# Optimization experiments

Measured on AMD Instinct MI355X. Metric: run time of the kernel, lower is better.

The kernel has to match this reference:

```python
import jax, jax.numpy as jnp
import numpy as np

B, S, V, H, NL, NH, FF, L = 32, 256, 30522, 768, 12, 12, 3072, 9
DH = H // NH
SCALE = 1.0 / float(np.sqrt(DH))

def _ln(x, g, b, eps=1e-12):
    mu = x.mean(-1, keepdims=True)
    var = ((x - mu) ** 2).mean(-1, keepdims=True)
    return (x - mu) * jax.lax.rsqrt(var + eps) * g + b

def _crf_nll(em, tags, mask, start, end, trans):
    # em: [B,S,L] log-softmaxed emissions; tags: [B,S] int; mask: [B,S] bool
    b, s, l = em.shape
    bi = jnp.arange(b)
    em_t = jnp.swapaxes(em, 0, 1)          # [S,B,L]
    tg_t = tags.T                           # [S,B]
    m_t = mask.T.astype(em.dtype)           # [S,B]
    # numerator: score of the gold path
    score0 = start[tags[:, 0]] + em[bi, 0, tags[:, 0]]
    def num_step(sc, xs):
        e, tg, tgp, m = xs
        return sc + m * (trans[tgp, tg] + e[bi, tg]), None
    num, _ = jax.lax.scan(num_step, score0, (em_t[1:], tg_t[1:], tg_t[:-1], m_t[1:]))
    seq_ends = mask.sum(1).astype(jnp.int32) - 1
    num = num + end[tags[bi, seq_ends]]
    # denominator: log partition via forward algorithm
    alpha0 = start[None, :] + em[:, 0]      # [B,L]
    def den_step(al, xs):
        e, m = xs
        new = jax.nn.logsumexp(al[:, :, None] + trans[None] + e[:, None, :], axis=1)
        return jnp.where(m[:, None] > 0, new, al), None
    alpha, _ = jax.lax.scan(den_step, alpha0, (em_t[1:], m_t[1:]))
    den = jax.nn.logsumexp(alpha + end[None, :], axis=1)
    return -(num - den).sum()   # torchcrf reduction='sum', negated in module

def _bert_crf_loss(token_ids, token_type_ids, attention_mask, y, p):
    b, s = token_ids.shape
    h = p['word_emb'][token_ids] + p['pos_emb'][:s][None] + p['type_emb'][token_type_ids]
    h = _ln(h, p['emb_ln_g'], p['emb_ln_b'])
    bias = (1.0 - attention_mask.astype(jnp.float32))[:, None, None, :] * -1e9
    def layer(hc, lp):
        Wq, bq, Wk, bk, Wv, bv, Wo, bo, g1, bln1, W1, b1, W2, b2, g2, bln2 = lp
        q = (hc @ Wq + bq).reshape(b, s, NH, DH)
        k = (hc @ Wk + bk).reshape(b, s, NH, DH)
        v = (hc @ Wv + bv).reshape(b, s, NH, DH)
        att = jnp.einsum('bqhd,bkhd->bhqk', q, k) * SCALE + bias
        att = jax.nn.softmax(att, axis=-1)
        ctx = jnp.einsum('bhqk,bkhd->bqhd', att, v).reshape(b, s, H)
        hc = _ln(hc + ctx @ Wo + bo, g1, bln1)
        ff = jax.nn.gelu(hc @ W1 + b1) @ W2 + b2
        hc = _ln(hc + ff, g2, bln2)
        return hc, None
    stacked = (p['Wq'], p['bq'], p['Wk'], p['bk'], p['Wv'], p['bv'], p['Wo'], p['bo'],
               p['ln1_g'], p['ln1_b'], p['W1'], p['b1'], p['W2'], p['b2'], p['ln2_g'], p['ln2_b'])
    h, _ = jax.lax.scan(layer, h, stacked)
    # dropout is identity in eval; fc has no bias; LogSoftmax over labels
    logits = jax.nn.log_softmax(h @ p['fc_w'], axis=-1)   # [B,S,L]
    return _crf_nll(logits, y, attention_mask.astype(bool), p['crf_start'], p['crf_end'], p['crf_trans'])

def setup_inputs() -> dict:
    key = jax.random.key(0)
    ks = iter(jax.random.split(key, 32))
    def nrm(shape, scale=0.02):
        return (jax.random.normal(next(ks), shape, jnp.float32) * scale)
    inp = dict(
        token_ids=jax.random.randint(next(ks), (B, S), 0, V),
        token_type_ids=jnp.zeros((B, S), jnp.int32),
        attention_mask=jnp.ones((B, S), jnp.int32),
        y=jax.random.randint(next(ks), (B, S), 0, L),
        word_emb=nrm((V, H)), pos_emb=nrm((S, H)), type_emb=nrm((2, H)),
        emb_ln_g=jnp.ones(H, jnp.float32), emb_ln_b=jnp.zeros(H, jnp.float32),
        Wq=nrm((NL, H, H)), bq=jnp.zeros((NL, H), jnp.float32),
        Wk=nrm((NL, H, H)), bk=jnp.zeros((NL, H), jnp.float32),
        Wv=nrm((NL, H, H)), bv=jnp.zeros((NL, H), jnp.float32),
        Wo=nrm((NL, H, H)), bo=jnp.zeros((NL, H), jnp.float32),
        ln1_g=jnp.ones((NL, H), jnp.float32), ln1_b=jnp.zeros((NL, H), jnp.float32),
        W1=nrm((NL, H, FF)), b1=jnp.zeros((NL, FF), jnp.float32),
        W2=nrm((NL, FF, H)), b2=jnp.zeros((NL, H), jnp.float32),
        ln2_g=jnp.ones((NL, H), jnp.float32), ln2_b=jnp.zeros((NL, H), jnp.float32),
        fc_w=nrm((H, L)),
        crf_start=nrm((L,), 0.1), crf_end=nrm((L,), 0.1), crf_trans=nrm((L, L), 0.1),
    )
    return inp

def reference(token_ids, token_type_ids, attention_mask, y, word_emb, pos_emb, type_emb,
              emb_ln_g, emb_ln_b, Wq, bq, Wk, bk, Wv, bv, Wo, bo, ln1_g, ln1_b,
              W1, b1, W2, b2, ln2_g, ln2_b, fc_w, crf_start, crf_end, crf_trans):
    p = dict(word_emb=word_emb, pos_emb=pos_emb, type_emb=type_emb,
             emb_ln_g=emb_ln_g, emb_ln_b=emb_ln_b, Wq=Wq, bq=bq, Wk=Wk, bk=bk,
             Wv=Wv, bv=bv, Wo=Wo, bo=bo, ln1_g=ln1_g, ln1_b=ln1_b,
             W1=W1, b1=b1, W2=W2, b2=b2, ln2_g=ln2_g, ln2_b=ln2_b,
             fc_w=fc_w, crf_start=crf_start, crf_end=crf_end, crf_trans=crf_trans)
    return _bert_crf_loss(token_ids, token_type_ids, attention_mask, y, p)
```

## Files before the change

### kernel.cpp

```cpp
#include <hip/hip_runtime.h>
#include <math.h>

typedef unsigned short ushortT;
typedef unsigned char u8;
typedef __attribute__((ext_vector_type(4))) float f32x4;
typedef __attribute__((ext_vector_type(4))) unsigned int u32x4;
typedef __attribute__((ext_vector_type(4))) unsigned short u16x4;
typedef __attribute__((ext_vector_type(4))) int i32x4;
typedef __attribute__((ext_vector_type(8))) __bf16 bf16x8;

namespace {
constexpr int S = 256;
constexpr int H = 768;
constexpr int NLAY = 12;
constexpr int NHD = 12;
constexpr int FF = 3072;
constexpr int LBL = 9;
constexpr int DH = 64;
constexpr int BATCH = 32;
constexpr int TOKENS = BATCH * S;
constexpr int QKVN = 3 * H;
constexpr float C2 = 0.18033688011112042f;

constexpr size_t HB_OFF  = 0;
constexpr size_t QB_OFF  = HB_OFF + (size_t)TOKENS*H/2;
constexpr size_t KB_OFF  = QB_OFF + (size_t)TOKENS*H/2;
constexpr size_t VT_OFF  = KB_OFF + (size_t)TOKENS*H/2;
constexpr size_t BIG_OFF = VT_OFF + (size_t)TOKENS*H/2;
constexpr size_t WTQ_OFF = BIG_OFF + (size_t)TOKENS*FF/2;
constexpr size_t WTO_OFF = WTQ_OFF + 3*(size_t)H*H/2;
constexpr size_t WT1_OFF = WTO_OFF + (size_t)H*H/2;
constexpr size_t WT2_OFF = WT1_OFF + (size_t)H*FF/2;
constexpr size_t EM_OFF  = WT2_OFF + (size_t)H*FF/2;
constexpr size_t PART_OFF= EM_OFF + (size_t)TOKENS*LBL;
constexpr size_t BQKV_OFF= PART_OFF + 64;
constexpr size_t H8_OFF  = BQKV_OFF + (size_t)NLAY*QKVN;
constexpr size_t WS_FLOATS = H8_OFF + (size_t)TOKENS*H/4;
}

__device__ __forceinline__ ushortT f2bf(float x) {
    unsigned u = __builtin_bit_cast(unsigned, x);
    u += 0x7fffu + ((u >> 16) & 1u);
    return (ushortT)(u >> 16);
}
__device__ __forceinline__ float bf2f(ushortT h) {
    unsigned u = ((unsigned)h) << 16;
    return __builtin_bit_cast(float, u);
}
__device__ __forceinline__ u8 f2fp8(float x) {
    return (u8)(__builtin_amdgcn_cvt_pk_fp8_f32(x, x, 0, false) & 0xff);
}
__device__ __forceinline__ unsigned f2fp8x4(float a, float b, float c, float d) {
    int p = __builtin_amdgcn_cvt_pk_fp8_f32(a, b, 0, false);
    p = __builtin_amdgcn_cvt_pk_fp8_f32(c, d, p, true);
    return (unsigned)p;
}

__device__ __forceinline__ float exp2i(float x) {
    float r; asm("v_exp_f32 %0, %1" : "=v"(r) : "v"(x)); return r;
}
__device__ __forceinline__ float log2i(float x) {
    float r; asm("v_log_f32 %0, %1" : "=v"(r) : "v"(x)); return r;
}

__device__ __forceinline__ float gelu_tanh(float x) {
    float u = 0.7978845608028654f * (x + 0.044715f * x * x * x);
    float t = exp2i(-2.8853900817779268f * u);
    return x / (1.0f + t);
}

__device__ __forceinline__ f32x4 mfma16(u32x4 a, u32x4 b, f32x4 c) {
    return __builtin_amdgcn_mfma_f32_16x16x32_bf16(
        __builtin_bit_cast(bf16x8, a), __builtin_bit_cast(bf16x8, b), c, 0, 0, 0);
}

__device__ __forceinline__ void gload_lds16(const ushortT* g, ushortT* l) {
    __builtin_amdgcn_global_load_lds(
        (const __attribute__((address_space(1))) unsigned int*)g,
        (__attribute__((address_space(3))) unsigned int*)l,
        16, 0, 0);
}
__device__ __forceinline__ void gload_lds16b(const u8* g, u8* l) {
    __builtin_amdgcn_global_load_lds(
        (const __attribute__((address_space(1))) unsigned int*)g,
        (__attribute__((address_space(3))) unsigned int*)l,
        16, 0, 0);
}

template<int MODE>
__global__ __launch_bounds__(256) void gemm_fp8(
    const u8* __restrict__ A, int lda,
    const u8* __restrict__ Bt, int ldb,
    const float* __restrict__ bias,
    void* __restrict__ Cv, int ldc, int K)
{
    __shared__ __align__(16) u8 As[3][128 * 64];
    __shared__ __align__(16) u8 Bs[3][128 * 64];
    const int tid = threadIdx.x;
    const int wave = tid >> 6, lane = tid & 63;

    int bxi = blockIdx.x, byi = blockIdx.y;
    {
        const int nwg = gridDim.x * gridDim.y;
        const int lin = byi * gridDim.x + bxi;
        const int cpx = nwg >> 3;
        const int sw = (lin & 7) * cpx + (lin >> 3);
        byi = sw / gridDim.x; bxi = sw - byi * gridDim.x;
    }
    const int bm = byi * 128, bn = bxi * 128;
    const u8* Ab = A + (size_t)bm * lda;
    const u8* Bb = Bt + (size_t)bn * ldb;
    const int wm = wave >> 1, wn = wave & 1;

    const int lrow = lane >> 2;
    const int lswb = ((lane & 3) ^ ((lrow >> 1) & 3)) * 16;
    const int rl = lane & 15;
    const int kg = lane >> 4;
    const int kg4 = kg << 2;
    const int key = (rl >> 1) & 3;
    const int kgh = kg >> 1, kgl8 = (kg & 1) * 8;

    f32x4 acc[4][4];
#pragma unroll
    for (int i = 0; i < 4; ++i)
#pragma unroll
        for (int j = 0; j < 4; ++j) acc[i][j] = (f32x4){0.f, 0.f, 0.f, 0.f};

    auto stage = [&](int buf, int kt) {
#pragma unroll
        for (int j = 0; j < 2; ++j) {
            int chunk = j * 4 + wave;
            gload_lds16b(Ab + (size_t)(chunk * 16 + lrow) * lda + kt * 64 + lswb,
                         &As[buf][chunk * 1024]);
        }
#pragma unroll
        for (int j = 0; j < 2; ++j) {
            int chunk = j * 4 + wave;
            gload_lds16b(Bb + (size_t)(chunk * 16 + lrow) * ldb + kt * 64 + lswb,
                         &Bs[buf][chunk * 1024]);
        }
    };

    const int nt = K >> 6;
    stage(0, 0);
    stage(1, (nt > 1) ? 1 : 0);
    int cur = 0;
    for (int t = 0; t < nt; ++t) {
        asm volatile("s_waitcnt vmcnt(4)" ::: "memory");
        __builtin_amdgcn_s_barrier();
        __builtin_amdgcn_sched_barrier(0);
#pragma unroll
        for (int ks = 0; ks < 2; ++ks) {
            long a[4], b[4];
#pragma unroll
            for (int mf = 0; mf < 4; ++mf)
                a[mf] = *(const long*)&As[cur][(wm * 64 + mf * 16 + rl) * 64 +
                                               (((ks * 2 + kgh) ^ key) << 4) + kgl8];
#pragma unroll
            for (int nf = 0; nf < 4; ++nf)
                b[nf] = *(const long*)&Bs[cur][(wn * 64 + nf * 16 + rl) * 64 +
                                               (((ks * 2 + kgh) ^ key) << 4) + kgl8];
            if (ks == 0) {
                const int nx = (t + 2 < nt) ? t + 2 : nt - 1;
                int nb = cur + 2; if (nb >= 3) nb -= 3;
                stage(nb, nx);
            }
#pragma unroll
            for (int mf = 0; mf < 4; ++mf)
#pragma unroll
                for (int nf = 0; nf < 4; ++nf)
                    acc[mf][nf] = __builtin_amdgcn_mfma_f32_16x16x32_fp8_fp8(
                        a[mf], b[nf], acc[mf][nf], 0, 0, 0);
        }
        cur = (cur + 1 == 3) ? 0 : cur + 1;
    }
    asm volatile("s_waitcnt vmcnt(0)" ::: "memory");

#pragma unroll
    for (int nf = 0; nf < 4; ++nf) {
        const int gn = bn + wn * 64 + nf * 16 + rl;
        const float bv = bias[gn];
#pragma unroll
        for (int mf = 0; mf < 4; ++mf) {
            const int gm = bm + wm * 64 + mf * 16 + kg4;
            if constexpr (MODE == 7) {
                u8* C8 = (u8*)Cv;
#pragma unroll
                for (int r = 0; r < 4; ++r)
                    C8[(size_t)(gm + r) * ldc + gn] = f2fp8(gelu_tanh(acc[mf][nf][r] + bv));
            } else {
                ushortT* Ch = (ushortT*)Cv;
#pragma unroll
                for (int r = 0; r < 4; ++r)
                    Ch[(size_t)(gm + r) * ldc + gn] = f2bf(acc[mf][nf][r] + bv);
            }
        }
    }
}

template<int WM, int WN, int MODE>
__global__ __launch_bounds__(256) void gemm_mfma(
    const ushortT* __restrict__ A, int lda, long long sAo, long long sAi,
    const ushortT* __restrict__ Bt, int ldb, long long sBo, long long sBi,
    const float* __restrict__ bias,
    void* __restrict__ Cv, int ldc, long long sCo, long long sCi,
    int K, int innerN)
{
    constexpr int BM = WM * 64, BN = WN * 64;
    __shared__ __align__(16) ushortT As[3][BM * 32];
    __shared__ __align__(16) ushortT Bs[3][BN * 32];
    const int tid = threadIdx.x;
    const int wave = tid >> 6, lane = tid & 63;
    const int ob = blockIdx.z / innerN, ib = blockIdx.z - ob * innerN;

    int bxi = blockIdx.x, byi = blockIdx.y;
    if (gridDim.z == 1) {
        const int nwg = gridDim.x * gridDim.y;
        const int lin = byi * gridDim.x + bxi;
        const int cpx = nwg >> 3;
        const int sw = (lin & 7) * cpx + (lin >> 3);
        byi = sw / gridDim.x; bxi = sw - byi * gridDim.x;
    }
    const int bm = byi * BM, bn = bxi * BN;
    const ushortT* Ab = A + ob * sAo + ib * sAi + (size_t)bm * lda;
    const ushortT* Bb = Bt + ob * sBo + ib * sBi + (size_t)bn * ldb;
    const int wm = wave / WN, wn = wave - wm * WN;

    const int lrow = lane >> 2;
    const int lsw16 = ((lane & 3) ^ ((lrow >> 1) & 3)) * 8;
    const int rl = lane & 15;
    const int kg4 = (lane >> 4) << 2;
    const int ksw = ((lane >> 4) ^ ((rl >> 1) & 3)) << 3;

    f32x4 acc[4][4];
#pragma unroll
    for (int i = 0; i < 4; ++i)
#pragma unroll
        for (int j = 0; j < 4; ++j) acc[i][j] = (f32x4){0.f, 0.f, 0.f, 0.f};

    auto stage = [&](int buf, int k0) {
#pragma unroll
        for (int j = 0; j < WM; ++j) {
            int chunk = j * 4 + wave;
            gload_lds16(Ab + (size_t)(chunk * 16 + lrow) * lda + k0 + lsw16,
                        &As[buf][chunk * 512]);
        }
#pragma unroll
        for (int j = 0; j < WN; ++j) {
            int chunk = j * 4 + wave;
            gload_lds16(Bb + (size_t)(chunk * 16 + lrow) * ldb + k0 + lsw16,
                        &Bs[buf][chunk * 512]);
        }
    };

    const int nt = K >> 5;
    stage(0, 0);
    stage(1, ((nt > 1) ? 1 : 0) << 5);
    int cur = 0;
    for (int t = 0; t < nt; ++t) {
        if constexpr (WM + WN == 4)
            asm volatile("s_waitcnt vmcnt(4)" ::: "memory");
        else
            asm volatile("s_waitcnt vmcnt(5)" ::: "memory");
        __builtin_amdgcn_s_barrier();
        __builtin_amdgcn_sched_barrier(0);
        u32x4 a[4], b[4];
#pragma unroll
        for (int mf = 0; mf < 4; ++mf)
            a[mf] = *(const u32x4*)&As[cur][(wm * 64 + mf * 16 + rl) * 32 + ksw];
#pragma unroll
        for (int nf = 0; nf < 4; ++nf)
            b[nf] = *(const u32x4*)&Bs[cur][(wn * 64 + nf * 16 + rl) * 32 + ksw];
        {
            const int nx = (t + 2 < nt) ? t + 2 : nt - 1;
            int nb = cur + 2; if (nb >= 3) nb -= 3;
            stage(nb, nx << 5);
        }
#pragma unroll
        for (int mf = 0; mf < 4; ++mf)
#pragma unroll
            for (int nf = 0; nf < 4; ++nf)
                acc[mf][nf] = mfma16(a[mf], b[nf], acc[mf][nf]);
        cur = (cur + 1 == 3) ? 0 : cur + 1;
    }
    asm volatile("s_waitcnt vmcnt(0)" ::: "memory");

    ushortT* Ch = (ushortT*)Cv + ob * sCo + ib * sCi;
    if constexpr (MODE == 6) {
        __shared__ float red6[2][4][64];
        const int* mrow = (const int*)bias + ob * S;
        float mb[4];
#pragma unroll
        for (int nf = 0; nf < 4; ++nf)
            mb[nf] = mrow[bn + wn * 64 + nf * 16 + rl] ? 0.f : -8e9f;
        float pm[4][4];
#pragma unroll
        for (int mf = 0; mf < 4; ++mf)
#pragma unroll
            for (int r = 0; r < 4; ++r) pm[mf][r] = -1e30f;
#pragma unroll
        for (int mf = 0; mf < 4; ++mf)
#pragma unroll
            for (int nf = 0; nf < 4; ++nf)
#pragma unroll
                for (int r = 0; r < 4; ++r) {
                    acc[mf][nf][r] += mb[nf];
                    pm[mf][r] = fmaxf(pm[mf][r], acc[mf][nf][r]);
                }
#pragma unroll
        for (int mf = 0; mf < 4; ++mf)
#pragma unroll
            for (int r = 0; r < 4; ++r) {
                float v = pm[mf][r];
                v = fmaxf(v, __shfl_xor(v, 1));
                v = fmaxf(v, __shfl_xor(v, 2));
                v = fmaxf(v, __shfl_xor(v, 4));
                v = fmaxf(v, __shfl_xor(v, 8));
                pm[mf][r] = v;
            }
        if (rl == 0) {
#pragma unroll
            for (int mf = 0; mf < 4; ++mf)
#pragma unroll
                for (int r = 0; r < 4; ++r)
                    red6[0][wn][mf * 16 + kg4 + r] = pm[mf][r];
        }
        __syncthreads();
        float Mx[4][4];
#pragma unroll
        for (int mf = 0; mf < 4; ++mf)
#pragma unroll
            for (int r = 0; r < 4; ++r) {
                const int row = mf * 16 + kg4 + r;
                Mx[mf][r] = fmaxf(fmaxf(red6[0][0][row], red6[0][1][row]),
                                  fmaxf(red6[0][2][row], red6[0][3][row]));
            }
        float ps[4][4];
#pragma unroll
        for (int mf = 0; mf < 4; ++mf)
#pragma unroll
            for (int r = 0; r < 4; ++r) ps[mf][r] = 0.f;
#pragma unroll
        for (int mf = 0; mf < 4; ++mf)
#pragma unroll
            for (int nf = 0; nf < 4; ++nf)
#pragma unroll
                for (int r = 0; r < 4; ++r) {
                    float e = exp2i(C2 * (acc[mf][nf][r] - Mx[mf][r]));
                    acc[mf][nf][r] = e;
                    ps[mf][r] += e;
                }
#pragma unroll
        for (int mf = 0; mf < 4; ++mf)
#pragma unroll
            for (int r = 0; r < 4; ++r) {
                float v = ps[mf][r];
                v += __shfl_xor(v, 1);
                v += __shfl_xor(v, 2);
                v += __shfl_xor(v, 4);
                v += __shfl_xor(v, 8);
                ps[mf][r] = v;
            }
        if (rl == 0) {
#pragma unroll
            for (int mf = 0; mf < 4; ++mf)
#pragma unroll
                for (int r = 0; r < 4; ++r)
                    red6[1][wn][mf * 16 + kg4 + r] = ps[mf][r];
        }
        __syncthreads();
#pragma unroll
        for (int mf = 0; mf < 4; ++mf) {
            float inv[4];
#pragma unroll
            for (int r = 0; r < 4; ++r) {
                const int row = mf * 16 + kg4 + r;
                inv[r] = 1.0f / (red6[1][0][row] + red6[1][1][row] +
                                 red6[1][2][row] + red6[1][3][row]);
            }
#pragma unroll
            for (int nf = 0; nf < 4; ++nf) {
                const int gn = bn + wn * 64 + nf * 16 + rl;
                const int gm = bm + mf * 16 + kg4;
#pragma unroll
                for (int r = 0; r < 4; ++r)
                    Ch[(size_t)(gm + r) * ldc + gn] = f2bf(acc[mf][nf][r] * inv[r]);
            }
        }
    } else {
#pragma unroll
        for (int nf = 0; nf < 4; ++nf) {
            int gn = bn + wn * 64 + nf * 16 + rl;
            float bv = 0.f;
            if constexpr (MODE != 4) bv = bias[gn];
#pragma unroll
            for (int mf = 0; mf < 4; ++mf) {
                int gm = bm + wm * 64 + mf * 16 + kg4;
                if constexpr (MODE == 5) {
                    const int region = gn / H;
                    const int col = gn - region * H;
                    if (region < 2) {
                        ushortT* o = (ushortT*)Cv + (size_t)region * TOKENS * H;
#pragma unroll
                        for (int r = 0; r < 4; ++r)
                            o[(size_t)(gm + r) * H + col] = f2bf(acc[mf][nf][r] + bv);
                    } else {
                        u16x4 o;
#pragma unroll
                        for (int r = 0; r < 4; ++r) o[r] = f2bf(acc[mf][nf][r] + bv);
                        const int b_ = gm >> 8, s0 = gm & 255;
                        const int h_ = col >> 6, dh = col & 63;
                        *(u16x4*)((ushortT*)Cv + 2 * (size_t)TOKENS * H +
                                  (((size_t)(b_ * NHD + h_) * DH + dh) << 8) + s0) = o;
                    }
                } else {
#pragma unroll
                    for (int r = 0; r < 4; ++r) {
                        float x = acc[mf][nf][r] + bv;
                        Ch[(size_t)(gm + r) * ldc + gn] = f2bf(x);
                    }
                }
            }
        }
    }
}

__global__ __launch_bounds__(256) void transpose_all_k(
    const float* __restrict__ Wq, const float* __restrict__ Wk,
    const float* __restrict__ Wv, const float* __restrict__ Wo,
    const float* __restrict__ W1, const float* __restrict__ W2,
    ushortT* __restrict__ wtqkv, ushortT* __restrict__ wto,
    u8* __restrict__ wt1, u8* __restrict__ wt2)
{
    int idx = blockIdx.x;
    const float* W; int R, C, tr, tc; int kind;
    ushortT* WTb = nullptr; u8* WT8 = nullptr;
    if (idx < 2304) {
        int mat = idx / 576, t = idx - mat * 576;
        tr = t / 24; tc = t - tr * 24; R = 768; C = 768; kind = 0;
        W = mat == 0 ? Wq : mat == 1 ? Wk : mat == 2 ? Wv : Wo;
        WTb = mat < 3 ? wtqkv + (size_t)mat * 768 * 768 : wto;
    } else if (idx < 4608) {
        int t = idx - 2304; tr = t / 96; tc = t - tr * 96;
        R = 768; C = 3072; W = W1; WT8 = wt1; kind = 1;
    } else {
        int t = idx - 4608; tr = t / 24; tc = t - tr * 24;
        R = 3072; C = 768; W = W2; WT8 = wt2; kind = 1;
    }
    int r0 = tr * 32, c0 = tc * 32;
    __shared__ float tl[32][33];
    int trd = threadIdx.x >> 3;
    int tc4 = (threadIdx.x & 7) * 4;
    const float4 v = *(const float4*)(W + (size_t)(r0 + trd) * C + c0 + tc4);
    tl[trd][tc4 + 0] = v.x; tl[trd][tc4 + 1] = v.y;
    tl[trd][tc4 + 2] = v.z; tl[trd][tc4 + 3] = v.w;
    __syncthreads();
    if (kind == 0) {
        u16x4 o;
#pragma unroll
        for (int q = 0; q < 4; ++q) o[q] = f2bf(tl[tc4 + q][trd]);
        *(u16x4*)(WTb + (size_t)(c0 + trd) * R + r0 + tc4) = o;
    } else {
        unsigned p = f2fp8x4(tl[tc4 + 0][trd], tl[tc4 + 1][trd],
                             tl[tc4 + 2][trd], tl[tc4 + 3][trd]);
        *(unsigned*)(WT8 + (size_t)(c0 + trd) * R + r0 + tc4) = p;
    }
}

__global__ __launch_bounds__(256) void pack_bias_k(
    const float* __restrict__ bq, const float* __restrict__ bk,
    const float* __restrict__ bv, float* __restrict__ out)
{
    int l = blockIdx.x / 3, r = blockIdx.x - (blockIdx.x / 3) * 3;
    const float* src = r == 0 ? bq : r == 1 ? bk : bv;
#pragma unroll
    for (int j = 0; j < 3; ++j) {
        int d = threadIdx.x + 256 * j;
        out[(size_t)l * QKVN + r * H + d] = src[(size_t)l * H + d];
    }
}

__global__ __launch_bounds__(256) void embed_ln_k(
    const int* __restrict__ ids, const int* __restrict__ tts,
    const float* __restrict__ wemb, const float* __restrict__ pemb,
    const float* __restrict__ temb, const float* __restrict__ g,
    const float* __restrict__ bp, ushortT* __restrict__ hb)
{
    const int tok = blockIdx.x * 4 + (threadIdx.x >> 6);
    const int lane = threadIdx.x & 63;
    const int d0 = lane * 12;
    const int spos = tok & (S - 1);
    const int id = ids[tok], tt = tts[tok];
    const float* wr = wemb + (size_t)id * H + d0;
    const float* pr = pemb + (size_t)spos * H + d0;
    const float* tr = temb + (size_t)tt * H + d0;
    float x[12]; float s = 0.f, ss = 0.f;
#pragma unroll
    for (int j = 0; j < 3; ++j) {
        float4 a = *(const float4*)(wr + j * 4);
        float4 b = *(const float4*)(pr + j * 4);
        float4 c = *(const float4*)(tr + j * 4);
        float v0 = a.x + b.x + c.x, v1 = a.y + b.y + c.y;
        float v2 = a.z + b.z + c.z, v3 = a.w + b.w + c.w;
        x[j*4+0] = v0; x[j*4+1] = v1; x[j*4+2] = v2; x[j*4+3] = v3;
        s += v0 + v1 + v2 + v3;
        ss += v0*v0 + v1*v1 + v2*v2 + v3*v3;
    }
#pragma unroll
    for (int m = 32; m; m >>= 1) { s += __shfl_xor(s, m); ss += __shfl_xor(ss, m); }
    float mu = s * (1.f / H);
    float var = ss * (1.f / H) - mu * mu;
    float rs = rsqrtf(var + 1e-12f);
#pragma unroll
    for (int j = 0; j < 3; ++j) {
        float4 gv = *(const float4*)(g + d0 + j * 4);
        float4 bv = *(const float4*)(bp + d0 + j * 4);
        u16x4 o;
        o[0] = f2bf((x[j*4+0] - mu) * rs * gv.x + bv.x);
        o[1] = f2bf((x[j*4+1] - mu) * rs * gv.y + bv.y);
        o[2] = f2bf((x[j*4+2] - mu) * rs * gv.z + bv.z);
        o[3] = f2bf((x[j*4+3] - mu) * rs * gv.w + bv.w);
        *(u16x4*)(hb + (size_t)tok * H + d0 + j * 4) = o;
    }
}

__global__ __launch_bounds__(256) void add_ln_k(
    ushortT* __restrict__ hb, const ushortT* __restrict__ add,
    const float* __restrict__ g, const float* __restrict__ bp,
    u8* __restrict__ h8)
{
    const int tok = blockIdx.x * 4 + (threadIdx.x >> 6);
    const int lane = threadIdx.x & 63;
    const int d0 = lane * 12;
    const size_t base = (size_t)tok * H + d0;
    float x[12]; float s = 0.f, ss = 0.f;
#pragma unroll
    for (int j = 0; j < 3; ++j) {
        u16x4 hv = *(const u16x4*)(hb + base + j * 4);
        u16x4 av = *(const u16x4*)(add + base + j * 4);
#pragma unroll
        for (int q = 0; q < 4; ++q) {
            float v = bf2f(hv[q]) + bf2f(av[q]);
            x[j*4+q] = v; s += v; ss += v * v;
        }
    }
#pragma unroll
    for (int m = 32; m; m >>= 1) { s += __shfl_xor(s, m); ss += __shfl_xor(ss, m); }
    float mu = s * (1.f / H);
    float var = ss * (1.f / H) - mu * mu;
    float rs = rsqrtf(var + 1e-12f);
#pragma unroll
    for (int j = 0; j < 3; ++j) {
        float4 gv = *(const float4*)(g + d0 + j * 4);
        float4 bv = *(const float4*)(bp + d0 + j * 4);
        float y0 = (x[j*4+0] - mu) * rs * gv.x + bv.x;
        float y1 = (x[j*4+1] - mu) * rs * gv.y + bv.y;
        float y2 = (x[j*4+2] - mu) * rs * gv.z + bv.z;
        float y3 = (x[j*4+3] - mu) * rs * gv.w + bv.w;
        u16x4 o;
        o[0] = f2bf(y0); o[1] = f2bf(y1); o[2] = f2bf(y2); o[3] = f2bf(y3);
        *(u16x4*)(hb + base + j * 4) = o;
        *(unsigned*)(h8 + base + j * 4) = f2fp8x4(y0, y1, y2, y3);
    }
}

__global__ __launch_bounds__(256) void logits_k(
    const ushortT* __restrict__ hb, const float* __restrict__ fcw,
    float* __restrict__ em)
{
    int tok = blockIdx.x, tid = threadIdx.x;
    float p[LBL];
#pragma unroll
    for (int l = 0; l < LBL; ++l) p[l] = 0.f;
    const ushortT* hr = hb + (size_t)tok * H;
#pragma unroll
    for (int j = 0; j < 3; ++j) {
        int d = tid + 256 * j;
        float hv = bf2f(hr[d]);
        const float* fr = fcw + (size_t)d * LBL;
#pragma unroll
        for (int l = 0; l < LBL; ++l) p[l] = fmaf(hv, fr[l], p[l]);
    }
    __shared__ float ls[4][LBL];
    __shared__ float lg[LBL];
    __shared__ float lse;
#pragma unroll
    for (int l = 0; l < LBL; ++l) {
        float v = p[l];
#pragma unroll
        for (int m = 32; m; m >>= 1) v += __shfl_xor(v, m);
        if ((tid & 63) == 0) ls[tid >> 6][l] = v;
    }
    __syncthreads();
    if (tid < LBL) lg[tid] = ls[0][tid] + ls[1][tid] + ls[2][tid] + ls[3][tid];
    __syncthreads();
    if (tid == 0) {
        float mx = lg[0];
#pragma unroll
        for (int j = 1; j < LBL; ++j) mx = fmaxf(mx, lg[j]);
        float sm = 0.f;
#pragma unroll
        for (int j = 0; j < LBL; ++j) sm += expf(lg[j] - mx);
        lse = mx + logf(sm);
    }
    __syncthreads();
    if (tid < LBL) em[(size_t)tok * LBL + tid] = lg[tid] - lse;
}

__global__ __launch_bounds__(64) void crf_k(
    const float* __restrict__ em, const int* __restrict__ tags,
    const int* __restrict__ mask, const float* __restrict__ sp,
    const float* __restrict__ ep, const float* __restrict__ trans,
    float* __restrict__ partial)
{
    constexpr float LOG2E = 1.4426950408889634f;
    constexpr float LN2   = 0.6931471805599453f;
    int b = blockIdx.x, t = threadIdx.x;
    __shared__ float eml[S * LBL];
    __shared__ int mkl[S];
    const float* emb = em + (size_t)b * S * LBL;
    const int* tg = tags + (size_t)b * S;
    const int* mk = mask + (size_t)b * S;

    for (int i = t * 4; i < S * LBL; i += 256) {
        float4 v = *(const float4*)&emb[i];
        v.x *= LOG2E; v.y *= LOG2E; v.z *= LOG2E; v.w *= LOG2E;
        *(float4*)&eml[i] = v;
    }
    *(i32x4*)&mkl[t * 4] = *(const i32x4*)&mk[t * 4];

    int cnt = 0; float ns = 0.f;
    for (int i = t; i < S; i += 64) {
        int m = mk[i];
        cnt += (m != 0);
        if (i >= 1 && m)
            ns += trans[tg[i - 1] * LBL + tg[i]] + emb[(size_t)i * LBL + tg[i]];
    }
#pragma unroll
    for (int m = 32; m; m >>= 1) { cnt += __shfl_xor(cnt, m); ns += __shfl_xor(ns, m); }
    float num = ns + sp[tg[0]] + emb[tg[0]] + ep[tg[cnt - 1]];

    int tt = t < LBL ? t : 0;
    float trc2[LBL];
#pragma unroll
    for (int i = 0; i < LBL; ++i) trc2[i] = trans[i * LBL + tt] * LOG2E;

    __syncthreads();

    float alpha2 = (t < LBL) ? sp[t] * LOG2E + eml[t] : -1e30f;
    for (int step = 1; step < S; ++step) {
        float av[LBL];
#pragma unroll
        for (int i = 0; i < LBL; ++i) av[i] = __shfl(alpha2, i) + trc2[i];
        float mx = av[0];
#pragma unroll
        for (int i = 1; i < LBL; ++i) mx = fmaxf(mx, av[i]);
        float sm = 0.f;
#pragma unroll
        for (int i = 0; i < LBL; ++i) sm += exp2i(av[i] - mx);
        float na = mx + log2i(sm) + eml[step * LBL + tt];
        alpha2 = (mkl[step] && t < LBL) ? na : alpha2;
    }
    float z = (t < LBL) ? alpha2 + ep[t] * LOG2E : -1e30f;
    float mx = z;
#pragma unroll
    for (int m = 8; m; m >>= 1) mx = fmaxf(mx, __shfl_xor(mx, m));
    float sm = exp2i(z - mx);
#pragma unroll
    for (int m = 8; m; m >>= 1) sm += __shfl_xor(sm, m);
    if (t == 0) partial[b] = (mx + log2i(sm)) * LN2 - num;
}

__global__ void finalize_k(const float* __restrict__ partial, float* __restrict__ out) {
    float s = 0.f;
    for (int i = 0; i < BATCH; ++i) s += partial[i];
    out[0] = s;
}

__global__ void sentinel_k(float* out) { out[0] = -12345.0f; }

extern "C" void kernel_launch(void* const* d_in, const int* in_sizes, int n_in,
                              void* d_out, int out_size, void* d_ws, size_t ws_size,
                              hipStream_t stream) {
    (void)in_sizes; (void)n_in; (void)out_size;
    const int* token_ids  = (const int*)d_in[0];
    const int* token_type = (const int*)d_in[1];
    const int* amask      = (const int*)d_in[2];
    const int* y          = (const int*)d_in[3];
    const float* wemb = (const float*)d_in[4];
    const float* pemb = (const float*)d_in[5];
    const float* temb = (const float*)d_in[6];
    const float* eg   = (const float*)d_in[7];
    const float* eb   = (const float*)d_in[8];
    const float* Wq = (const float*)d_in[9];
    const float* bq = (const float*)d_in[10];
    const float* Wk = (const float*)d_in[11];
    const float* bk = (const float*)d_in[12];
    const float* Wv = (const float*)d_in[13];
    const float* bv = (const float*)d_in[14];
    const float* Wo = (const float*)d_in[15];
    const float* bo = (const float*)d_in[16];
    const float* ln1g = (const float*)d_in[17];
    const float* ln1b = (const float*)d_in[18];
    const float* W1 = (const float*)d_in[19];
    const float* b1 = (const float*)d_in[20];
    const float* W2 = (const float*)d_in[21];
    const float* b2 = (const float*)d_in[22];
    const float* ln2g = (const float*)d_in[23];
    const float* ln2b = (const float*)d_in[24];
    const float* fcw = (const float*)d_in[25];
    const float* crf_s = (const float*)d_in[26];
    const float* crf_e = (const float*)d_in[27];
    const float* crf_t = (const float*)d_in[28];

    if (ws_size < WS_FLOATS * sizeof(float)) {
        sentinel_k<<<1, 1, 0, stream>>>((float*)d_out);
        return;
    }

    float* ws = (float*)d_ws;
    ushortT* hb   = (ushortT*)(ws + HB_OFF);
    ushortT* qb   = (ushortT*)(ws + QB_OFF);
    ushortT* kb   = (ushortT*)(ws + KB_OFF);
    ushortT* vt   = (ushortT*)(ws + VT_OFF);
    ushortT* big  = (ushortT*)(ws + BIG_OFF);
    u8*      big8 = (u8*)(ws + BIG_OFF);
    ushortT* wtq  = (ushortT*)(ws + WTQ_OFF);
    ushortT* wto  = (ushortT*)(ws + WTO_OFF);
    u8*      wt1  = (u8*)(ws + WT1_OFF);
    u8*      wt2  = (u8*)(ws + WT2_OFF);
    float*   embuf = ws + EM_OFF;
    float*   part  = ws + PART_OFF;
    float*   bqkv  = ws + BQKV_OFF;
    u8*      h8    = (u8*)(ws + H8_OFF);

    pack_bias_k<<<NLAY * 3, 256, 0, stream>>>(bq, bk, bv, bqkv);
    embed_ln_k<<<TOKENS / 4, 256, 0, stream>>>(token_ids, token_type, wemb, pemb,
                                               temb, eg, eb, hb);

    constexpr long long HH = (long long)H * H;
    constexpr long long HF = (long long)H * FF;
    constexpr long long TOKH = (long long)S * H;
    constexpr long long ATT_B = (long long)NHD * S * S;
    constexpr long long ATT_H = (long long)S * S;
    constexpr long long VT_B = (long long)NHD * DH * S;
    constexpr long long VT_H = (long long)DH * S;

    dim3 gQKV(QKVN / 128, TOKENS / 128, 1);
    dim3 gProj(H / 128, TOKENS / 128, 1);
    dim3 gFF1(FF / 128, TOKENS / 128, 1);
    dim3 gScores(1, S / 64, BATCH * NHD);
    dim3 gPV(1, 1, BATCH * NHD);

    for (int l = 0; l < NLAY; ++l) {
        transpose_all_k<<<6912, 256, 0, stream>>>(
            Wq + l * HH, Wk + l * HH, Wv + l * HH, Wo + l * HH,
            W1 + l * HF, W2 + l * HF, wtq, wto, wt1, wt2);

        gemm_mfma<2,2,5><<<gQKV, 256, 0, stream>>>(
            hb, H, 0, 0, wtq, H, 0, 0, bqkv + (size_t)l * QKVN,
            qb, H, 0, 0, H, 1);

        gemm_mfma<1,4,6><<<gScores, 256, 0, stream>>>(
            qb, H, TOKH, DH, kb, H, TOKH, DH, (const float*)amask,
            big, S, ATT_B, ATT_H, DH, NHD);

        gemm_mfma<4,1,4><<<gPV, 256, 0, stream>>>(
            big, S, ATT_B, ATT_H, vt, S, VT_B, VT_H, nullptr,
            qb, H, TOKH, DH, S, NHD);

        gemm_mfma<2,2,0><<<gProj, 256, 0, stream>>>(
            qb, H, 0, 0, wto, H, 0, 0, bo + l * H, kb, H, 0, 0, H, 1);

        add_ln_k<<<TOKENS / 4, 256, 0, stream>>>(hb, kb, ln1g + l * H, ln1b + l * H, h8);

        gemm_fp8<7><<<gFF1, 256, 0, stream>>>(
            h8, H, wt1, H, b1 + (long long)l * FF, big8, FF, H);

        gemm_fp8<8><<<gProj, 256, 0, stream>>>(
            big8, FF, wt2, FF, b2 + l * H, qb, H, FF);

        add_ln_k<<<TOKENS / 4, 256, 0, stream>>>(hb, qb, ln2g + l * H, ln2b + l * H, h8);
    }

    logits_k<<<TOKENS, 256, 0, stream>>>(hb, fcw, embuf);
    crf_k<<<BATCH, 64, 0, stream>>>(embuf, y, amask, crf_s, crf_e, crf_t, part);
    finalize_k<<<1, 1, 0, stream>>>(part, (float*)d_out);
}
```

Measured before the change: 2.767 ms.

## Run QKV and output projection GEMMs in FP8 instead of BF16

Moves the QKV projection and attention output projection from the BF16 MFMA GEMM to the FP8 GEMM path. Weights for Wq/Wk/Wv/Wo are now transposed straight to FP8, the embedding LN also writes an FP8 copy of the hidden state, and the PV GEMM writes its context output as FP8 to feed the output projection. A new FP8 GEMM epilogue mode does the Q/K/V scatter, and the tile-swizzle remapping is removed from the BF16 GEMM. The aim is to double MFMA throughput and halve the operand bytes on these GEMMs, at the cost of lower precision in the attention projections and a possible loss of L2 locality from dropping the swizzle.

```diff
diff --git a/kernel.cpp b/kernel.cpp
--- a/kernel.cpp
+++ b/kernel.cpp
@@ -28,14 +28,15 @@
 constexpr size_t VT_OFF  = KB_OFF + (size_t)TOKENS*H/2;
 constexpr size_t BIG_OFF = VT_OFF + (size_t)TOKENS*H/2;
 constexpr size_t WTQ_OFF = BIG_OFF + (size_t)TOKENS*FF/2;
-constexpr size_t WTO_OFF = WTQ_OFF + 3*(size_t)H*H/2;
-constexpr size_t WT1_OFF = WTO_OFF + (size_t)H*H/2;
-constexpr size_t WT2_OFF = WT1_OFF + (size_t)H*FF/2;
-constexpr size_t EM_OFF  = WT2_OFF + (size_t)H*FF/2;
+constexpr size_t WTO_OFF = WTQ_OFF + 3*(size_t)H*H/4;
+constexpr size_t WT1_OFF = WTO_OFF + (size_t)H*H/4;
+constexpr size_t WT2_OFF = WT1_OFF + (size_t)H*FF/4;
+constexpr size_t EM_OFF  = WT2_OFF + (size_t)H*FF/4;
 constexpr size_t PART_OFF= EM_OFF + (size_t)TOKENS*LBL;
 constexpr size_t BQKV_OFF= PART_OFF + 64;
 constexpr size_t H8_OFF  = BQKV_OFF + (size_t)NLAY*QKVN;
-constexpr size_t WS_FLOATS = H8_OFF + (size_t)TOKENS*H/4;
+constexpr size_t CT8_OFF = H8_OFF + (size_t)TOKENS*H/4;
+constexpr size_t WS_FLOATS = CT8_OFF + (size_t)TOKENS*H/4;
 }
 
 __device__ __forceinline__ ushortT f2bf(float x) {
@@ -188,6 +189,23 @@
 #pragma unroll
                 for (int r = 0; r < 4; ++r)
                     C8[(size_t)(gm + r) * ldc + gn] = f2fp8(gelu_tanh(acc[mf][nf][r] + bv));
+            } else if constexpr (MODE == 9) {
+                const int region = gn / H;
+                const int col = gn - region * H;
+                if (region < 2) {
+                    ushortT* o = (ushortT*)Cv + (size_t)region * TOKENS * H;
+#pragma unroll
+                    for (int r = 0; r < 4; ++r)
+                        o[(size_t)(gm + r) * H + col] = f2bf(acc[mf][nf][r] + bv);
+                } else {
+                    u16x4 o;
+#pragma unroll
+                    for (int r = 0; r < 4; ++r) o[r] = f2bf(acc[mf][nf][r] + bv);
+                    const int b_ = gm >> 8, s0 = gm & 255;
+                    const int h_ = col >> 6, dh = col & 63;
+                    *(u16x4*)((ushortT*)Cv + 2 * (size_t)TOKENS * H +
+                              (((size_t)(b_ * NHD + h_) * DH + dh) << 8) + s0) = o;
+                }
             } else {
                 ushortT* Ch = (ushortT*)Cv;
 #pragma unroll
@@ -213,15 +231,7 @@
     const int wave = tid >> 6, lane = tid & 63;
     const int ob = blockIdx.z / innerN, ib = blockIdx.z - ob * innerN;
 
-    int bxi = blockIdx.x, byi = blockIdx.y;
-    if (gridDim.z == 1) {
-        const int nwg = gridDim.x * gridDim.y;
-        const int lin = byi * gridDim.x + bxi;
-        const int cpx = nwg >> 3;
-        const int sw = (lin & 7) * cpx + (lin >> 3);
-        byi = sw / gridDim.x; bxi = sw - byi * gridDim.x;
-    }
-    const int bm = byi * BM, bn = bxi * BN;
+    const int bm = blockIdx.y * BM, bn = blockIdx.x * BN;
     const ushortT* Ab = A + ob * sAo + ib * sAi + (size_t)bm * lda;
     const ushortT* Bb = Bt + ob * sBo + ib * sBi + (size_t)bn * ldb;
     const int wm = wave / WN, wn = wave - wm * WN;
@@ -285,8 +295,8 @@
     }
     asm volatile("s_waitcnt vmcnt(0)" ::: "memory");
 
-    ushortT* Ch = (ushortT*)Cv + ob * sCo + ib * sCi;
     if constexpr (MODE == 6) {
+        ushortT* Ch = (ushortT*)Cv + ob * sCo + ib * sCi;
         __shared__ float red6[2][4][64];
         const int* mrow = (const int*)bias + ob * S;
         float mb[4];
@@ -388,38 +398,16 @@
             }
         }
     } else {
+        u8* C8 = (u8*)Cv + ob * sCo + ib * sCi;
 #pragma unroll
         for (int nf = 0; nf < 4; ++nf) {
             int gn = bn + wn * 64 + nf * 16 + rl;
-            float bv = 0.f;
-            if constexpr (MODE != 4) bv = bias[gn];
 #pragma unroll
             for (int mf = 0; mf < 4; ++mf) {
                 int gm = bm + wm * 64 + mf * 16 + kg4;
-                if constexpr (MODE == 5) {
-                    const int region = gn / H;
-                    const int col = gn - region * H;
-                    if (region < 2) {
-                        ushortT* o = (ushortT*)Cv + (size_t)region * TOKENS * H;
-#pragma unroll
-                        for (int r = 0; r < 4; ++r)
-                            o[(size_t)(gm + r) * H + col] = f2bf(acc[mf][nf][r] + bv);
-                    } else {
-                        u16x4 o;
-#pragma unroll
-                        for (int r = 0; r < 4; ++r) o[r] = f2bf(acc[mf][nf][r] + bv);
-                        const int b_ = gm >> 8, s0 = gm & 255;
-                        const int h_ = col >> 6, dh = col & 63;
-                        *(u16x4*)((ushortT*)Cv + 2 * (size_t)TOKENS * H +
-                                  (((size_t)(b_ * NHD + h_) * DH + dh) << 8) + s0) = o;
-                    }
-                } else {
-#pragma unroll
-                    for (int r = 0; r < 4; ++r) {
-                        float x = acc[mf][nf][r] + bv;
-                        Ch[(size_t)(gm + r) * ldc + gn] = f2bf(x);
-                    }
-                }
+#pragma unroll
+                for (int r = 0; r < 4; ++r)
+                    C8[(size_t)(gm + r) * ldc + gn] = f2fp8(acc[mf][nf][r]);
             }
         }
     }
@@ -429,23 +417,22 @@
     const float* __restrict__ Wq, const float* __restrict__ Wk,
     const float* __restrict__ Wv, const float* __restrict__ Wo,
     const float* __restrict__ W1, const float* __restrict__ W2,
-    ushortT* __restrict__ wtqkv, ushortT* __restrict__ wto,
+    u8* __restrict__ wtqkv8, u8* __restrict__ wto8,
     u8* __restrict__ wt1, u8* __restrict__ wt2)
 {
     int idx = blockIdx.x;
-    const float* W; int R, C, tr, tc; int kind;
-    ushortT* WTb = nullptr; u8* WT8 = nullptr;
+    const float* W; int R, C, tr, tc; u8* WT8;
     if (idx < 2304) {
         int mat = idx / 576, t = idx - mat * 576;
-        tr = t / 24; tc = t - tr * 24; R = 768; C = 768; kind = 0;
+        tr = t / 24; tc = t - tr * 24; R = 768; C = 768;
         W = mat == 0 ? Wq : mat == 1 ? Wk : mat == 2 ? Wv : Wo;
-        WTb = mat < 3 ? wtqkv + (size_t)mat * 768 * 768 : wto;
+        WT8 = mat < 3 ? wtqkv8 + (size_t)mat * 768 * 768 : wto8;
     } else if (idx < 4608) {
         int t = idx - 2304; tr = t / 96; tc = t - tr * 96;
-        R = 768; C = 3072; W = W1; WT8 = wt1; kind = 1;
+        R = 768; C = 3072; W = W1; WT8 = wt1;
     } else {
         int t = idx - 4608; tr = t / 24; tc = t - tr * 24;
-        R = 3072; C = 768; W = W2; WT8 = wt2; kind = 1;
+        R = 3072; C = 768; W = W2; WT8 = wt2;
     }
     int r0 = tr * 32, c0 = tc * 32;
     __shared__ float tl[32][33];
@@ -455,16 +442,9 @@
     tl[trd][tc4 + 0] = v.x; tl[trd][tc4 + 1] = v.y;
     tl[trd][tc4 + 2] = v.z; tl[trd][tc4 + 3] = v.w;
     __syncthreads();
-    if (kind == 0) {
-        u16x4 o;
-#pragma unroll
-        for (int q = 0; q < 4; ++q) o[q] = f2bf(tl[tc4 + q][trd]);
-        *(u16x4*)(WTb + (size_t)(c0 + trd) * R + r0 + tc4) = o;
-    } else {
-        unsigned p = f2fp8x4(tl[tc4 + 0][trd], tl[tc4 + 1][trd],
-                             tl[tc4 + 2][trd], tl[tc4 + 3][trd]);
-        *(unsigned*)(WT8 + (size_t)(c0 + trd) * R + r0 + tc4) = p;
-    }
+    unsigned p = f2fp8x4(tl[tc4 + 0][trd], tl[tc4 + 1][trd],
+                         tl[tc4 + 2][trd], tl[tc4 + 3][trd]);
+    *(unsigned*)(WT8 + (size_t)(c0 + trd) * R + r0 + tc4) = p;
 }
 
 __global__ __launch_bounds__(256) void pack_bias_k(
@@ -484,7 +464,7 @@
     const int* __restrict__ ids, const int* __restrict__ tts,
     const float* __restrict__ wemb, const float* __restrict__ pemb,
     const float* __restrict__ temb, const float* __restrict__ g,
-    const float* __restrict__ bp, ushortT* __restrict__ hb)
+    const float* __restrict__ bp, ushortT* __restrict__ hb, u8* __restrict__ h8)
 {
     const int tok = blockIdx.x * 4 + (threadIdx.x >> 6);
     const int lane = threadIdx.x & 63;
@@ -515,12 +495,14 @@
     for (int j = 0; j < 3; ++j) {
         float4 gv = *(const float4*)(g + d0 + j * 4);
         float4 bv = *(const float4*)(bp + d0 + j * 4);
+        float y0 = (x[j*4+0] - mu) * rs * gv.x + bv.x;
+        float y1 = (x[j*4+1] - mu) * rs * gv.y + bv.y;
+        float y2 = (x[j*4+2] - mu) * rs * gv.z + bv.z;
+        float y3 = (x[j*4+3] - mu) * rs * gv.w + bv.w;
         u16x4 o;
-        o[0] = f2bf((x[j*4+0] - mu) * rs * gv.x + bv.x);
-        o[1] = f2bf((x[j*4+1] - mu) * rs * gv.y + bv.y);
-        o[2] = f2bf((x[j*4+2] - mu) * rs * gv.z + bv.z);
-        o[3] = f2bf((x[j*4+3] - mu) * rs * gv.w + bv.w);
+        o[0] = f2bf(y0); o[1] = f2bf(y1); o[2] = f2bf(y2); o[3] = f2bf(y3);
         *(u16x4*)(hb + (size_t)tok * H + d0 + j * 4) = o;
+        *(unsigned*)(h8 + (size_t)tok * H + d0 + j * 4) = f2fp8x4(y0, y1, y2, y3);
     }
 }
 
@@ -719,24 +701,25 @@
     }
 
     float* ws = (float*)d_ws;
-    ushortT* hb   = (ushortT*)(ws + HB_OFF);
-    ushortT* qb   = (ushortT*)(ws + QB_OFF);
-    ushortT* kb   = (ushortT*)(ws + KB_OFF);
-    ushortT* vt   = (ushortT*)(ws + VT_OFF);
-    ushortT* big  = (ushortT*)(ws + BIG_OFF);
-    u8*      big8 = (u8*)(ws + BIG_OFF);
-    ushortT* wtq  = (ushortT*)(ws + WTQ_OFF);
-    ushortT* wto  = (ushortT*)(ws + WTO_OFF);
-    u8*      wt1  = (u8*)(ws + WT1_OFF);
-    u8*      wt2  = (u8*)(ws + WT2_OFF);
+    ushortT* hb    = (ushortT*)(ws + HB_OFF);
+    ushortT* qb    = (ushortT*)(ws + QB_OFF);
+    ushortT* kb    = (ushortT*)(ws + KB_OFF);
+    ushortT* vt    = (ushortT*)(ws + VT_OFF);
+    ushortT* big   = (ushortT*)(ws + BIG_OFF);
+    u8*      big8  = (u8*)(ws + BIG_OFF);
+    u8*      wtq8  = (u8*)(ws + WTQ_OFF);
+    u8*      wto8  = (u8*)(ws + WTO_OFF);
+    u8*      wt1   = (u8*)(ws + WT1_OFF);
+    u8*      wt2   = (u8*)(ws + WT2_OFF);
     float*   embuf = ws + EM_OFF;
     float*   part  = ws + PART_OFF;
     float*   bqkv  = ws + BQKV_OFF;
     u8*      h8    = (u8*)(ws + H8_OFF);
+    u8*      ctx8  = (u8*)(ws + CT8_OFF);
 
     pack_bias_k<<<NLAY * 3, 256, 0, stream>>>(bq, bk, bv, bqkv);
     embed_ln_k<<<TOKENS / 4, 256, 0, stream>>>(token_ids, token_type, wemb, pemb,
-                                               temb, eg, eb, hb);
+                                               temb, eg, eb, hb, h8);
 
     constexpr long long HH = (long long)H * H;
     constexpr long long HF = (long long)H * FF;
@@ -755,22 +738,21 @@
     for (int l = 0; l < NLAY; ++l) {
         transpose_all_k<<<6912, 256, 0, stream>>>(
             Wq + l * HH, Wk + l * HH, Wv + l * HH, Wo + l * HH,
-            W1 + l * HF, W2 + l * HF, wtq, wto, wt1, wt2);
-
-        gemm_mfma<2,2,5><<<gQKV, 256, 0, stream>>>(
-            hb, H, 0, 0, wtq, H, 0, 0, bqkv + (size_t)l * QKVN,
-            qb, H, 0, 0, H, 1);
+            W1 + l * HF, W2 + l * HF, wtq8, wto8, wt1, wt2);
+
+        gemm_fp8<9><<<gQKV, 256, 0, stream>>>(
+            h8, H, wtq8, H, bqkv + (size_t)l * QKVN, qb, H, H);
 
         gemm_mfma<1,4,6><<<gScores, 256, 0, stream>>>(
             qb, H, TOKH, DH, kb, H, TOKH, DH, (const float*)amask,
             big, S, ATT_B, ATT_H, DH, NHD);
 
-        gemm_mfma<4,1,4><<<gPV, 256, 0, stream>>>(
+        gemm_mfma<4,1,10><<<gPV, 256, 0, stream>>>(
             big, S, ATT_B, ATT_H, vt, S, VT_B, VT_H, nullptr,
-            qb, H, TOKH, DH, S, NHD);
-
-        gemm_mfma<2,2,0><<<gProj, 256, 0, stream>>>(
-            qb, H, 0, 0, wto, H, 0, 0, bo + l * H, kb, H, 0, 0, H, 1);
+            ctx8, H, TOKH, DH, S, NHD);
+
+        gemm_fp8<8><<<gProj, 256, 0, stream>>>(
+            ctx8, H, wto8, H, bo + l * H, kb, H, H);
 
         add_ln_k<<<TOKENS / 4, 256, 0, stream>>>(hb, kb, ln1g + l * H, ln1b + l * H, h8);
 
```

New measurement: 2.585 ms. -6.6%, faster.
